# Optimization experiments

Measured on AMD Instinct MI355X. Metric: run time of the kernel, lower is better.

Reference implementation:

```python
import jax, jax.numpy as jnp
import numpy as np

TEMPERATURE = 0.2

def setup_inputs() -> dict:
    key = jax.random.key(0)
    k1, k2 = jax.random.split(key)
    B, D = 4096, 128
    emb_i = jax.random.normal(k1, (B, D), dtype=jnp.float32)
    emb_j = jax.random.normal(k2, (B, D), dtype=jnp.float32)
    return {"emb_i": emb_i, "emb_j": emb_j}

def reference(emb_i, emb_j):
    # L2-normalize each embedding row, concat -> z: [2B, D]
    z_i = emb_i / jnp.linalg.norm(emb_i, axis=1, keepdims=True)
    z_j = emb_j / jnp.linalg.norm(emb_j, axis=1, keepdims=True)
    z = jnp.concatenate([z_i, z_j], axis=0)          # [2B, D]
    N2 = z.shape[0]
    N = N2 // 2
    # cosine similarity of normalized vectors == dot product
    sim = z @ z.T                                    # [2B, 2B]
    logits = sim / TEMPERATURE
    # denominator excludes only the diagonal (k != i)
    diag_mask = jnp.eye(N2, dtype=bool)
    masked = jnp.where(diag_mask, -jnp.inf, logits)
    lse = jax.nn.logsumexp(masked, axis=1)           # [2B]
    # positive pair for row i is i+N (mod 2N)
    pos_idx = jnp.concatenate([jnp.arange(N) + N, jnp.arange(N)])
    pos_logits = jnp.take_along_axis(logits, pos_idx[:, None], axis=1)[:, 0]
    # loss = (1/2N) * sum_i -log( exp(pos_i) / sum_{k!=i} exp(logits[i,k]) )
    loss = jnp.mean(lse - pos_logits)
    return loss
```

## Files before the change

### kernel.cpp

```cpp
#include <hip/hip_runtime.h>
#include <hip/hip_bf16.h>
#include <hip/hip_fp8.h>

typedef __attribute__((ext_vector_type(4))) float f32x4;
typedef long long i64;

#define EXP_SCALE 7.213475204444817f

__device__ __forceinline__ float fast_exp2(float x) {
#if __has_builtin(__builtin_amdgcn_exp2f)
  return __builtin_amdgcn_exp2f(x);
#else
  return exp2f(x);
#endif
}


__global__ __launch_bounds__(256) void k_normalize(
    const float* __restrict__ emb_i, const float* __restrict__ emb_j,
    unsigned char* __restrict__ z, float* __restrict__ rowsum,
    float* __restrict__ out)
{
  if (blockIdx.x == 0 && threadIdx.x == 0) out[0] = 0.0f;
  if (threadIdx.x < 16) rowsum[(blockIdx.x << 4) + threadIdx.x] = 0.0f;
  const int t = threadIdx.x;
  const int c = t >> 4;
  const int sub = t & 15;
  const int row = (blockIdx.x << 4) + c;
  const float* src = (row < 4096) ? (emb_i + row * 128) : (emb_j + (row - 4096) * 128);
  float4 v0 = reinterpret_cast<const float4*>(src)[sub * 2];
  float4 v1 = reinterpret_cast<const float4*>(src)[sub * 2 + 1];
  float ss = v0.x*v0.x + v0.y*v0.y + v0.z*v0.z + v0.w*v0.w
           + v1.x*v1.x + v1.y*v1.y + v1.z*v1.z + v1.w*v1.w;
  #pragma unroll
  for (int m = 1; m < 16; m <<= 1) ss += __shfl_xor(ss, m, 64);
  float rinv = 1.0f / sqrtf(ss);
  unsigned char st[8];
  st[0] = __hip_fp8_e4m3(v0.x * rinv).__x;
  st[1] = __hip_fp8_e4m3(v0.y * rinv).__x;
  st[2] = __hip_fp8_e4m3(v0.z * rinv).__x;
  st[3] = __hip_fp8_e4m3(v0.w * rinv).__x;
  st[4] = __hip_fp8_e4m3(v1.x * rinv).__x;
  st[5] = __hip_fp8_e4m3(v1.y * rinv).__x;
  st[6] = __hip_fp8_e4m3(v1.z * rinv).__x;
  st[7] = __hip_fp8_e4m3(v1.w * rinv).__x;
  unsigned char* dst = z + blockIdx.x * 2048 + (sub >> 2) * 512 +
                       (((sub & 3) << 4) + c) * 8;
  *reinterpret_cast<i64*>(dst) = *reinterpret_cast<i64*>(st);
}

__global__ __launch_bounds__(256, 4) void k_simlse(
    const unsigned char* __restrict__ z,
    float* __restrict__ rowsum,
    float* __restrict__ rowpos)
{
  const int w = threadIdx.x >> 6;
  const int lane = threadIdx.x & 63;
  const int q = lane >> 4;
  const int c = lane & 15;

  int ch = 0;
  while ((int)blockIdx.x >= 4 * (ch + 1) * (ch + 2)) ++ch;
  const int rb = blockIdx.x - 4 * ch * (ch + 1);
  const int R0 = rb << 6;
  const bool upper = (rb < (ch << 3));

  i64 a[4][4];
  {
    const unsigned char* ap = z + (R0 >> 4) * 2048 + (lane << 3);
    #pragma unroll
    for (int rg = 0; rg < 4; ++rg)
      #pragma unroll
      for (int kk = 0; kk < 4; ++kk)
        a[rg][kk] = *reinterpret_cast<const i64*>(ap + rg * 2048 + kk * 512);
  }

  float acc[4][4];
  #pragma unroll
  for (int rg = 0; rg < 4; ++rg)
    #pragma unroll
    for (int e = 0; e < 4; ++e) acc[rg][e] = 0.0f;
  float pacc[4] = {0.f, 0.f, 0.f, 0.f};
  float colp[8];
  #pragma unroll
  for (int i = 0; i < 8; ++i) colp[i] = 0.0f;

  __shared__ float lsum[4][64];
  __shared__ float lpos[4][16];

  const int ct0 = (ch << 5) + w;
  const unsigned char* bwave = z + ct0 * 2048 + (lane << 3);

  const int pos0t = ((R0 + 4096) & 8191) >> 4;
  const int ipb = ((pos0t >> 5) == ch) ? ((pos0t & 31) >> 2) : -99;

  i64 b0[4], b1[4];
  auto ldb = [&](i64 (&dst)[4], int idx) {
    const unsigned char* p = bwave + idx * 8192;
    dst[0] = *reinterpret_cast<const i64*>(p);
    dst[1] = *reinterpret_cast<const i64*>(p + 512);
    dst[2] = *reinterpret_cast<const i64*>(p + 1024);
    dst[3] = *reinterpret_cast<const i64*>(p + 1536);
  };

  auto process = [&](const i64 (&bb)[4], int i) {
    f32x4 cc[4];
    #pragma unroll
    for (int rr = 0; rr < 4; ++rr) cc[rr] = f32x4{0.f, 0.f, 0.f, 0.f};
    #pragma unroll
    for (int kk = 0; kk < 4; ++kk)
      #pragma unroll
      for (int rr = 0; rr < 4; ++rr)
        cc[rr] = __builtin_amdgcn_mfma_f32_16x16x32_fp8_fp8(
            a[rr][kk], bb[kk], cc[rr], 0, 0, 0);
    float cp0 = 0.0f, cp1 = 0.0f;
    #pragma unroll
    for (int rr = 0; rr < 4; ++rr)
      #pragma unroll
      for (int e = 0; e < 4; ++e) {
        float tv = fast_exp2(__builtin_fmaf(cc[rr][e], EXP_SCALE, -EXP_SCALE));
        acc[rr][e] += tv;
        if (upper) { if (rr & 1) cp1 += tv; else cp0 += tv; }
      }
    if (upper) colp[i] = cp0 + cp1;
    if (i == ipb) {
      #pragma unroll
      for (int rr = 0; rr < 4; ++rr) {
        if (rr == w) {
          #pragma unroll
          for (int e = 0; e < 4; ++e)
            if (c == ((q << 2) + e)) pacc[e] = cc[rr][e] * 5.0f;
        }
      }
    }
  };

  ldb(b0, 0);
  #pragma unroll 1
  for (int i = 0; i < 8; i += 2) {
    ldb(b1, i + 1);
    process(b0, i);
    if (i + 2 < 8) ldb(b0, i + 2);
    process(b1, i + 1);
  }

  if (upper) {
    #pragma unroll
    for (int i = 0; i < 8; ++i) {
      float v = colp[i];
      v += __shfl_xor(v, 16, 64);
      v += __shfl_xor(v, 32, 64);
      if (lane < 16)
        atomicAdd(&rowsum[((ct0 + (i << 2)) << 4) + c], v);
    }
  }

  #pragma unroll
  for (int m = 1; m < 16; m <<= 1) {
    #pragma unroll
    for (int rg = 0; rg < 4; ++rg)
      #pragma unroll
      for (int e = 0; e < 4; ++e)
        acc[rg][e] += __shfl_xor(acc[rg][e], m, 64);
    #pragma unroll
    for (int e = 0; e < 4; ++e) pacc[e] += __shfl_xor(pacc[e], m, 64);
  }

  if (c == 0) {
    #pragma unroll
    for (int rg = 0; rg < 4; ++rg)
      #pragma unroll
      for (int e = 0; e < 4; ++e)
        lsum[w][rg * 16 + (q << 2) + e] = acc[rg][e];
    #pragma unroll
    for (int e = 0; e < 4; ++e) lpos[w][(q << 2) + e] = pacc[e];
  }
  __syncthreads();

  if (threadIdx.x < 64) {
    const int t = threadIdx.x;
    float s = lsum[0][t] + lsum[1][t] + lsum[2][t] + lsum[3][t];
    atomicAdd(&rowsum[R0 + t], s);
    if (ipb != -99)
      rowpos[R0 + t] = lpos[t >> 4][t & 15];
  }
}

__global__ __launch_bounds__(256) void k_finish(
    const float* __restrict__ rowsum, const float* __restrict__ rowpos,
    float* __restrict__ out)
{
  const int r = blockIdx.x * 256 + threadIdx.x;
  float tot = rowsum[r] - 1.0f;
  float v = 5.0f + logf(tot) - rowpos[r & 4095];
  #pragma unroll
  for (int m = 1; m < 64; m <<= 1) v += __shfl_xor(v, m, 64);
  __shared__ float red[4];
  if ((threadIdx.x & 63) == 0) red[threadIdx.x >> 6] = v;
  __syncthreads();
  if (threadIdx.x == 0)
    atomicAdd(out, (red[0] + red[1] + red[2] + red[3]) * (1.0f / 8192.0f));
}

extern "C" void kernel_launch(void* const* d_in, const int* in_sizes, int n_in,
                              void* d_out, int out_size, void* d_ws, size_t ws_size,
                              hipStream_t stream) {
  const float* emb_i = (const float*)d_in[0];
  const float* emb_j = (const float*)d_in[1];
  unsigned char* z = (unsigned char*)d_ws;
  float* rowsum = (float*)((char*)d_ws + (1 << 20));
  float* rowpos = rowsum + 8192;
  float* out = (float*)d_out;

  k_normalize<<<512, 256, 0, stream>>>(emb_i, emb_j, z, rowsum, out);
  k_simlse<<<1088, 256, 0, stream>>>(z, rowsum, rowpos);
  k_finish<<<32, 256, 0, stream>>>(rowsum, rowpos, out);
}
```

Baseline: 76.14 us.

## Interleave fp8 K-chunks per lane for 16-byte loads and deepen B prefetch

```diff
diff --git a/kernel.cpp b/kernel.cpp
--- a/kernel.cpp
+++ b/kernel.cpp
@@ -3,6 +3,7 @@
 #include <hip/hip_fp8.h>
 
 typedef __attribute__((ext_vector_type(4))) float f32x4;
+typedef __attribute__((ext_vector_type(2))) long long i64x2;
 typedef long long i64;
 
 #define EXP_SCALE 7.213475204444817f
@@ -44,12 +45,12 @@
   st[5] = __hip_fp8_e4m3(v1.y * rinv).__x;
   st[6] = __hip_fp8_e4m3(v1.z * rinv).__x;
   st[7] = __hip_fp8_e4m3(v1.w * rinv).__x;
-  unsigned char* dst = z + blockIdx.x * 2048 + (sub >> 2) * 512 +
-                       (((sub & 3) << 4) + c) * 8;
+  unsigned char* dst = z + blockIdx.x * 2048 +
+                       (((sub & 3) << 4) + c) * 32 + (sub >> 2) * 8;
   *reinterpret_cast<i64*>(dst) = *reinterpret_cast<i64*>(st);
 }
 
-__global__ __launch_bounds__(256, 4) void k_simlse(
+__global__ __launch_bounds__(256, 3) void k_simlse(
     const unsigned char* __restrict__ z,
     float* __restrict__ rowsum,
     float* __restrict__ rowpos)
@@ -65,14 +66,14 @@
   const int R0 = rb << 6;
   const bool upper = (rb < (ch << 3));
 
-  i64 a[4][4];
+  i64x2 a2[4][2];
   {
-    const unsigned char* ap = z + (R0 >> 4) * 2048 + (lane << 3);
-    #pragma unroll
-    for (int rg = 0; rg < 4; ++rg)
-      #pragma unroll
-      for (int kk = 0; kk < 4; ++kk)
-        a[rg][kk] = *reinterpret_cast<const i64*>(ap + rg * 2048 + kk * 512);
+    const unsigned char* ap = z + (R0 >> 4) * 2048 + (lane << 5);
+    #pragma unroll
+    for (int rg = 0; rg < 4; ++rg) {
+      a2[rg][0] = *reinterpret_cast<const i64x2*>(ap + rg * 2048);
+      a2[rg][1] = *reinterpret_cast<const i64x2*>(ap + rg * 2048 + 16);
+    }
   }
 
   float acc[4][4];
@@ -89,21 +90,19 @@
   __shared__ float lpos[4][16];
 
   const int ct0 = (ch << 5) + w;
-  const unsigned char* bwave = z + ct0 * 2048 + (lane << 3);
+  const unsigned char* bwave = z + ct0 * 2048 + (lane << 5);
 
   const int pos0t = ((R0 + 4096) & 8191) >> 4;
   const int ipb = ((pos0t >> 5) == ch) ? ((pos0t & 31) >> 2) : -99;
 
-  i64 b0[4], b1[4];
-  auto ldb = [&](i64 (&dst)[4], int idx) {
+  i64x2 b0[2], b1[2], b2[2], b3[2];
+  auto ldb = [&](i64x2 (&dst)[2], int idx) {
     const unsigned char* p = bwave + idx * 8192;
-    dst[0] = *reinterpret_cast<const i64*>(p);
-    dst[1] = *reinterpret_cast<const i64*>(p + 512);
-    dst[2] = *reinterpret_cast<const i64*>(p + 1024);
-    dst[3] = *reinterpret_cast<const i64*>(p + 1536);
+    dst[0] = *reinterpret_cast<const i64x2*>(p);
+    dst[1] = *reinterpret_cast<const i64x2*>(p + 16);
   };
 
-  auto process = [&](const i64 (&bb)[4], int i) {
+  auto process = [&](const i64x2 (&bb)[2], int i) {
     f32x4 cc[4];
     #pragma unroll
     for (int rr = 0; rr < 4; ++rr) cc[rr] = f32x4{0.f, 0.f, 0.f, 0.f};
@@ -112,7 +111,7 @@
       #pragma unroll
       for (int rr = 0; rr < 4; ++rr)
         cc[rr] = __builtin_amdgcn_mfma_f32_16x16x32_fp8_fp8(
-            a[rr][kk], bb[kk], cc[rr], 0, 0, 0);
+            a2[rr][kk >> 1][kk & 1], bb[kk >> 1][kk & 1], cc[rr], 0, 0, 0);
     float cp0 = 0.0f, cp1 = 0.0f;
     #pragma unroll
     for (int rr = 0; rr < 4; ++rr)
@@ -135,14 +134,15 @@
     }
   };
 
-  ldb(b0, 0);
-  #pragma unroll 1
-  for (int i = 0; i < 8; i += 2) {
-    ldb(b1, i + 1);
-    process(b0, i);
-    if (i + 2 < 8) ldb(b0, i + 2);
-    process(b1, i + 1);
-  }
+  ldb(b0, 0); ldb(b1, 1); ldb(b2, 2); ldb(b3, 3);
+  process(b0, 0); ldb(b0, 4);
+  process(b1, 1); ldb(b1, 5);
+  process(b2, 2); ldb(b2, 6);
+  process(b3, 3); ldb(b3, 7);
+  process(b0, 4);
+  process(b1, 5);
+  process(b2, 6);
+  process(b3, 7);
 
   if (upper) {
     #pragma unroll
```

After: 80.50 us. +5.7%, slower.
